# Kernel tuning notes

Measured on AMD Instinct MI355X. Metric: run time of the kernel, lower is better.

The kernel has to match this reference:

```python
import jax, jax.numpy as jnp
import numpy as np

B_SZ, D, HW, STRIDE, HEADS, DK, DV = 32, 64, 64, 4, 2, 32, 32
N = HW * HW                      # 4096 query tokens
M = (HW // STRIDE) ** 2          # 256 key/value tokens
EPS = 1e-5


def setup_inputs() -> dict:
    key = jax.random.key(0)
    ks = jax.random.split(key, 8)
    w = lambda k, s: jax.random.normal(k, s, dtype=jnp.float32) * 0.02
    return {
        "x": jax.random.normal(ks[0], (B_SZ, D, HW, HW), dtype=jnp.float32),
        "W_dw": jax.random.normal(ks[1], (D, 1, STRIDE, STRIDE), dtype=jnp.float32) * 0.1,
        "b_dw": jnp.zeros((D,), jnp.float32),
        "Wq": w(ks[2], (HEADS * DK, D)), "bq": jnp.zeros((HEADS * DK,), jnp.float32),
        "Wk": w(ks[3], (HEADS * DK, D)), "bk": jnp.zeros((HEADS * DK,), jnp.float32),
        "Wv": w(ks[4], (HEADS * DV, D)), "bv": jnp.zeros((HEADS * DV,), jnp.float32),
        "Wo": w(ks[5], (D, HEADS * DV)), "bo": jnp.zeros((D,), jnp.float32),
        "B": jax.random.normal(ks[6], (1, HEADS, N, M), dtype=jnp.float32),
    }


def reference(x, W_dw, b_dw, Wq, bq, Wk, bk, Wv, bv, Wo, bo, B):
    b, c, h, w = x.shape
    heads = B.shape[1]
    dk = Wq.shape[0] // heads
    dv = Wv.shape[0] // heads
    s = W_dw.shape[-1]

    # LayerNorm over (C, H, W), no affine params
    mu = jnp.mean(x, axis=(1, 2, 3), keepdims=True)
    var = jnp.mean((x - mu) ** 2, axis=(1, 2, 3), keepdims=True)
    xn = (x - mu) * jax.lax.rsqrt(var + EPS)

    # Q from normalized input: (b, N, c)
    xr = jnp.transpose(xn.reshape(b, c, h * w), (0, 2, 1))
    q = (xr @ Wq.T + bq).reshape(b, h * w, heads, dk).transpose(0, 2, 1, 3)

    # K/V from depthwise-conv downsample of the *unnormalized* x (as in source)
    kc = jax.lax.conv_general_dilated(
        x, W_dw, window_strides=(s, s), padding="VALID",
        feature_group_count=c,
        dimension_numbers=("NCHW", "OIHW", "NCHW"),
    ) + b_dw[None, :, None, None]
    kh, kw = kc.shape[2], kc.shape[3]
    kv_in = jnp.transpose(kc.reshape(b, c, kh * kw), (0, 2, 1))  # (b, M, c)
    k = (kv_in @ Wk.T + bk).reshape(b, kh * kw, heads, dk).transpose(0, 2, 1, 3)
    v = (kv_in @ Wv.T + bv).reshape(b, kh * kw, heads, dv).transpose(0, 2, 1, 3)

    # Attention with additive relative bias
    attn = jnp.einsum("bhid,bhjd->bhij", q, k) * (dk ** -0.5) + B
    attn = jax.nn.softmax(attn, axis=-1)
    tmp = jnp.einsum("bhij,bhjd->bhid", attn, v)           # (b, heads, N, dv)
    tmp = tmp.transpose(0, 2, 1, 3).reshape(b, h * w, heads * dv)

    # Output proj; NOTE: source does a raw .view(b, d, h, w) (reshape, not permute)
    out = (tmp @ Wo.T + bo).reshape(b, c, h, w)
    return out + x
```

## Files before the change

kernel.cpp:

```cpp
#include <hip/hip_runtime.h>

typedef float f32x4 __attribute__((ext_vector_type(4)));

#define MFMA8(a, b, c) __builtin_amdgcn_mfma_f32_16x16x32_fp8_fp8((long)(a), (long)(b), (c), 0, 0, 0)

__device__ __forceinline__ unsigned char f2fp8(float v) {
    int pk = __builtin_amdgcn_cvt_pk_fp8_f32(v, v, 0, false);
    return (unsigned char)(pk & 0xff);
}
__device__ __forceinline__ long packrow8(const float* p) {
    f32x4 a = *(const f32x4*)(p);
    f32x4 b = *(const f32x4*)(p + 4);
    int lo = __builtin_amdgcn_cvt_pk_fp8_f32(a.x, a.y, 0, false);
    lo = __builtin_amdgcn_cvt_pk_fp8_f32(a.z, a.w, lo, true);
    int hi = __builtin_amdgcn_cvt_pk_fp8_f32(b.x, b.y, 0, false);
    hi = __builtin_amdgcn_cvt_pk_fp8_f32(b.z, b.w, hi, true);
    return (long)(((unsigned long)(unsigned int)hi << 32) | (unsigned int)lo);
}

__global__ __launch_bounds__(256) void k_ln_part(const float* __restrict__ x,
                                                 float* __restrict__ part) {
    const int chunk = blockIdx.x, b = blockIdx.y, t = threadIdx.x;
    const float4* p = (const float4*)(x + b * 262144 + chunk * 16384);
    float s = 0.f, ss = 0.f;
    #pragma unroll
    for (int r = 0; r < 16; ++r) {
        float4 v = p[r * 256 + t];
        s  += v.x + v.y + v.z + v.w;
        ss += v.x * v.x + v.y * v.y + v.z * v.z + v.w * v.w;
    }
    #pragma unroll
    for (int off = 32; off > 0; off >>= 1) {
        s  += __shfl_down(s, off);
        ss += __shfl_down(ss, off);
    }
    __shared__ float sm[8];
    int wv = t >> 6;
    if ((t & 63) == 0) { sm[wv * 2] = s; sm[wv * 2 + 1] = ss; }
    __syncthreads();
    if (t == 0) {
        float S  = sm[0] + sm[2] + sm[4] + sm[6];
        float SS = sm[1] + sm[3] + sm[5] + sm[7];
        part[(b * 16 + chunk) * 2]     = S;
        part[(b * 16 + chunk) * 2 + 1] = SS;
    }
}

__global__ void k_ln_fin(const float* __restrict__ part, float* __restrict__ stats) {
    int t = threadIdx.x;
    if (t < 32) {
        float S = 0.f, SS = 0.f;
        for (int k = 0; k < 16; ++k) {
            S  += part[(t * 16 + k) * 2];
            SS += part[(t * 16 + k) * 2 + 1];
        }
        const float inv = 1.0f / 262144.0f;
        float mu  = S * inv;
        float var = SS * inv - mu * mu;
        stats[t * 2]     = mu;
        stats[t * 2 + 1] = rsqrtf(var + 1e-5f);
    }
}

__global__ __launch_bounds__(512) void k_kvb(
    const float* __restrict__ x, const float* __restrict__ Wdw, const float* __restrict__ bdw,
    const float* __restrict__ Wk, const float* __restrict__ bk,
    const float* __restrict__ Wv, const float* __restrict__ bv,
    unsigned char* __restrict__ Kg, unsigned char* __restrict__ Vg)
{
    __shared__ __align__(16) unsigned char Y[16 * 72];
    const int mi = blockIdx.x, b = blockIdx.y;
    const int t = threadIdx.x, w = t >> 6, lane = t & 63;
    const int quad = lane >> 4, l = lane & 15;
    const float* xb = x + b * 262144;

    const int s2l = lane & 3, mjl = lane >> 2;
    #pragma unroll
    for (int ci = 0; ci < 8; ++ci) {
        int c = w * 8 + ci;
        float wd0 = Wdw[c * 16 + 0 + s2l];
        float wd1 = Wdw[c * 16 + 4 + s2l];
        float wd2 = Wdw[c * 16 + 8 + s2l];
        float wd3 = Wdw[c * 16 + 12 + s2l];
        const float* xr = xb + c * 4096 + mi * 256;
        float acc = xr[lane] * wd0;
        acc = fmaf(xr[64 + lane],  wd1, acc);
        acc = fmaf(xr[128 + lane], wd2, acc);
        acc = fmaf(xr[192 + lane], wd3, acc);
        acc += __shfl_xor(acc, 1);
        acc += __shfl_xor(acc, 2);
        if (s2l == 0) Y[mjl * 72 + c] = f2fp8(acc + bdw[c]);
    }
    __syncthreads();

    long ya0 = *(const long*)(Y + l * 72 + quad * 8);
    long ya1 = *(const long*)(Y + l * 72 + 32 + quad * 8);
    if (w < 4) {
        int e4 = w;
        long f0 = packrow8(Wk + (e4 * 16 + l) * 64 + quad * 8);
        long f1 = packrow8(Wk + (e4 * 16 + l) * 64 + 32 + quad * 8);
        float bb = bk[e4 * 16 + l];
        f32x4 c = { bb, bb, bb, bb };
        c = MFMA8(ya0, f0, c);
        c = MFMA8(ya1, f1, c);
        unsigned char* kd = Kg + b * 16384 + (mi * 16 + quad * 4) * 64 + e4 * 16 + l;
        #pragma unroll
        for (int r = 0; r < 4; ++r) kd[r * 64] = f2fp8(c[r]);
    } else {
        int d4 = w - 4;
        long f0 = packrow8(Wv + (d4 * 16 + l) * 64 + quad * 8);
        long f1 = packrow8(Wv + (d4 * 16 + l) * 64 + 32 + quad * 8);
        f32x4 c = { bv[d4 * 16 + quad * 4 + 0], bv[d4 * 16 + quad * 4 + 1],
                    bv[d4 * 16 + quad * 4 + 2], bv[d4 * 16 + quad * 4 + 3] };
        c = MFMA8(f0, ya0, c);
        c = MFMA8(f1, ya1, c);
        unsigned char* vd = Vg + b * 16384 + (d4 * 16 + quad * 4) * 256 + mi * 16 + l;
        #pragma unroll
        for (int r = 0; r < 4; ++r) vd[r * 256] = f2fp8(c[r]);
    }
}

__global__ __launch_bounds__(512, 4) void k_attn2(
    const float* __restrict__ x, const float* __restrict__ Wq, const float* __restrict__ bq,
    const float* __restrict__ Wo, const float* __restrict__ bo, const float* __restrict__ Bb,
    const float* __restrict__ stats, const unsigned char* __restrict__ Kg,
    const unsigned char* __restrict__ Vg, float* __restrict__ outp)
{
    __shared__ __align__(16) long smem8[7104];
    unsigned char* S = (unsigned char*)smem8;
    unsigned char* Kf = S;
    unsigned char* Vt = S + 20480;
    unsigned char* XS = S + 37888;
    unsigned char* QF = S + 42496;
    unsigned char* TS = S + 52224;
    const int tile = blockIdx.x, b = blockIdx.y;
    const int t = threadIdx.x, w = t >> 6, lane = t & 63;
    const int quad = lane >> 4, l = lane & 15;
    unsigned char* PS = S + 47104 + w * 640;
    const int n0 = tile * 64;
    const float mu = stats[2 * b], rstd = stats[2 * b + 1];
    const float* xb = x + b * 262144;
    const float SCALE = 0.17677669529663687f;

    const unsigned char* Kgb = Kg + b * 16384;
    const unsigned char* Vgb = Vg + b * 16384;
    #pragma unroll
    for (int r = 0; r < 2; ++r) {
        int idx = t + 512 * r;
        int m = idx >> 2, c16 = (idx & 3) * 16;
        *(uint4*)(Kf + m * 80 + c16) = *(const uint4*)(Kgb + m * 64 + c16);
        int d = idx >> 4, e16 = (idx & 15) * 16;
        *(uint4*)(Vt + d * 272 + e16) = *(const uint4*)(Vgb + d * 256 + e16);
    }
    #pragma unroll
    for (int ci = 0; ci < 8; ++ci) {
        int c = w * 8 + ci;
        float v = (xb[c * 4096 + n0 + lane] - mu) * rstd;
        XS[lane * 72 + c] = f2fp8(v);
    }
    const int rtq = w >> 1, ct0 = (w & 1) * 2;
    long wqF[4], woF[4];
    float bqr[2], bor[2];
    #pragma unroll
    for (int i = 0; i < 2; ++i) {
        #pragma unroll
        for (int st = 0; st < 2; ++st) {
            wqF[i * 2 + st] = packrow8(Wq + ((ct0 + i) * 16 + l) * 64 + st * 32 + quad * 8);
            woF[i * 2 + st] = packrow8(Wo + ((ct0 + i) * 16 + l) * 64 + st * 32 + quad * 8);
        }
        bqr[i] = bq[(ct0 + i) * 16 + l];
        bor[i] = bo[(ct0 + i) * 16 + l];
    }
    __syncthreads();

    {
        long xa0 = *(const long*)(XS + (rtq * 16 + l) * 72 + quad * 8);
        long xa1 = *(const long*)(XS + (rtq * 16 + l) * 72 + 32 + quad * 8);
        #pragma unroll
        for (int i = 0; i < 2; ++i) {
            f32x4 c = { bqr[i], bqr[i], bqr[i], bqr[i] };
            c = MFMA8(xa0, wqF[i * 2 + 0], c);
            c = MFMA8(xa1, wqF[i * 2 + 1], c);
            unsigned char* qd = QF + (rtq * 16 + quad * 4) * 72 + (ct0 + i) * 16 + l;
            #pragma unroll
            for (int r = 0; r < 4; ++r) qd[r * 72] = f2fp8(c[r]);
        }
    }
    __syncthreads();

    const int h = w & 1, nq = w >> 1;
    long qa = *(const long*)(QF + (nq * 16 + l) * 72 + h * 32 + quad * 8);
    f32x4 O0 = { 0, 0, 0, 0 }, O1 = { 0, 0, 0, 0 };
    float Lp[4] = { 0, 0, 0, 0 };
    const float* Bbase = Bb + h * 1048576 + (n0 + nq * 16 + quad * 4) * 256;

    #pragma unroll 2
    for (int mc = 0; mc < 8; ++mc) {
        float Bv[2][4];
        #pragma unroll
        for (int sub = 0; sub < 2; ++sub)
            #pragma unroll
            for (int r = 0; r < 4; ++r)
                Bv[sub][r] = Bbase[r * 256 + (mc * 2 + sub) * 16 + l];
        long kb0 = *(const long*)(Kf + ((mc * 2 + 0) * 16 + l) * 80 + h * 32 + quad * 8);
        long kb1 = *(const long*)(Kf + ((mc * 2 + 1) * 16 + l) * 80 + h * 32 + quad * 8);
        #pragma unroll
        for (int sub = 0; sub < 2; ++sub) {
            f32x4 sc = { 0, 0, 0, 0 };
            sc = MFMA8(qa, sub ? kb1 : kb0, sc);
            unsigned char* pw = PS + (quad * 4) * 40 + sub * 16 + l;
            #pragma unroll
            for (int r = 0; r < 4; ++r) {
                float p = __expf(fmaf(sc[r], SCALE, Bv[sub][r]));
                Lp[r] += p;
                pw[r * 40] = f2fp8(p);
            }
        }
        long pa  = *(const long*)(PS + l * 40 + quad * 8);
        long vb0 = *(const long*)(Vt + (h * 32 + l) * 272 + mc * 32 + quad * 8);
        long vb1 = *(const long*)(Vt + (h * 32 + 16 + l) * 272 + mc * 32 + quad * 8);
        O0 = MFMA8(pa, vb0, O0);
        O1 = MFMA8(pa, vb1, O1);
    }
    #pragma unroll
    for (int r = 0; r < 4; ++r) {
        #pragma unroll
        for (int d = 1; d < 16; d <<= 1) Lp[r] += __shfl_xor(Lp[r], d);
    }
    {
        unsigned char* td = TS + (nq * 16 + quad * 4) * 72 + h * 32 + l;
        #pragma unroll
        for (int r = 0; r < 4; ++r) {
            float inv = 1.0f / Lp[r];
            td[r * 72]      = f2fp8(O0[r] * inv);
            td[r * 72 + 16] = f2fp8(O1[r] * inv);
        }
    }
    __syncthreads();

    {
        long ta0 = *(const long*)(TS + (rtq * 16 + l) * 72 + quad * 8);
        long ta1 = *(const long*)(TS + (rtq * 16 + l) * 72 + 32 + quad * 8);
        float* ob = outp + b * 262144 + tile * 4096;
        const float* xr2 = xb + tile * 4096;
        #pragma unroll
        for (int i = 0; i < 2; ++i) {
            f32x4 c = { bor[i], bor[i], bor[i], bor[i] };
            c = MFMA8(ta0, woF[i * 2 + 0], c);
            c = MFMA8(ta1, woF[i * 2 + 1], c);
            #pragma unroll
            for (int r = 0; r < 4; ++r) {
                int off = (rtq * 16 + quad * 4 + r) * 64 + (ct0 + i) * 16 + l;
                ob[off] = c[r] + xr2[off];
            }
        }
    }
}

__global__ __launch_bounds__(512) void k_fused(
    const float* __restrict__ x, const float* __restrict__ Wdw, const float* __restrict__ bdw,
    const float* __restrict__ Wq, const float* __restrict__ bq,
    const float* __restrict__ Wk, const float* __restrict__ bk,
    const float* __restrict__ Wv, const float* __restrict__ bv,
    const float* __restrict__ Wo, const float* __restrict__ bo,
    const float* __restrict__ Bb, const float* __restrict__ stats,
    float* __restrict__ outp)
{
    __shared__ long smem8[6784];
    unsigned char* S = (unsigned char*)smem8;
    unsigned char* Kf = S;
    unsigned char* Vt = S + 18432;
    unsigned char* Y  = S + 35328;
    unsigned char* XS = S + 35328;
    unsigned char* QF = S + 35328 + 4608;
    unsigned char* TS = S + 35328 + 14336;

    const int tg = blockIdx.x, b = blockIdx.y;
    const int t = threadIdx.x, w = t >> 6, lane = t & 63;
    const int quad = lane >> 4, l = lane & 15;
    unsigned char* PS = S + 35328 + 9216 + w * 640;

    const float mu = stats[2 * b], rstd = stats[2 * b + 1];
    const float* xb = x + b * 262144;
    const float SCALE = 0.17677669529663687f;

    long wkF[8], wvF[8];
    #pragma unroll
    for (int e4 = 0; e4 < 4; ++e4)
        #pragma unroll
        for (int st = 0; st < 2; ++st) {
            wkF[e4 * 2 + st] = packrow8(Wk + (e4 * 16 + l) * 64 + st * 32 + quad * 8);
            wvF[e4 * 2 + st] = packrow8(Wv + (e4 * 16 + l) * 64 + st * 32 + quad * 8);
        }
    const int rtq = w >> 1, ct0 = (w & 1) * 2;
    long wqF[4], woF[4];
    #pragma unroll
    for (int i = 0; i < 2; ++i)
        #pragma unroll
        for (int st = 0; st < 2; ++st) {
            wqF[i * 2 + st] = packrow8(Wq + ((ct0 + i) * 16 + l) * 64 + st * 32 + quad * 8);
            woF[i * 2 + st] = packrow8(Wo + ((ct0 + i) * 16 + l) * 64 + st * 32 + quad * 8);
        }
    float bkr[4], bvr[4][4], bqr[2], bor[2];
    #pragma unroll
    for (int e4 = 0; e4 < 4; ++e4) bkr[e4] = bk[e4 * 16 + l];
    #pragma unroll
    for (int d4 = 0; d4 < 4; ++d4)
        #pragma unroll
        for (int r = 0; r < 4; ++r) bvr[d4][r] = bv[d4 * 16 + quad * 4 + r];
    #pragma unroll
    for (int i = 0; i < 2; ++i) { bqr[i] = bq[(ct0 + i) * 16 + l]; bor[i] = bo[(ct0 + i) * 16 + l]; }

    {
        const int s2l = lane & 3, mjl = lane >> 2;
        for (int ci = 0; ci < 8; ++ci) {
            int c = w * 8 + ci;
            float wd0 = Wdw[c * 16 + 0 + s2l];
            float wd1 = Wdw[c * 16 + 4 + s2l];
            float wd2 = Wdw[c * 16 + 8 + s2l];
            float wd3 = Wdw[c * 16 + 12 + s2l];
            float bdc = bdw[c];
            #pragma unroll 4
            for (int mi = 0; mi < 16; ++mi) {
                const float* xr = xb + c * 4096 + mi * 256;
                float acc = xr[lane] * wd0;
                acc = fmaf(xr[64 + lane],  wd1, acc);
                acc = fmaf(xr[128 + lane], wd2, acc);
                acc = fmaf(xr[192 + lane], wd3, acc);
                acc += __shfl_xor(acc, 1);
                acc += __shfl_xor(acc, 2);
                if (s2l == 0) Y[(mi * 16 + mjl) * 72 + c] = f2fp8(acc + bdc);
            }
        }
    }
    __syncthreads();

    #pragma unroll
    for (int i = 0; i < 2; ++i) {
        int rt = w * 2 + i;
        long ya0 = *(const long*)(Y + (rt * 16 + l) * 72 + quad * 8);
        long ya1 = *(const long*)(Y + (rt * 16 + l) * 72 + 32 + quad * 8);
        #pragma unroll
        for (int e4 = 0; e4 < 4; ++e4) {
            f32x4 c = { bkr[e4], bkr[e4], bkr[e4], bkr[e4] };
            c = MFMA8(ya0, wkF[e4 * 2 + 0], c);
            c = MFMA8(ya1, wkF[e4 * 2 + 1], c);
            unsigned char* kd = Kf + (rt * 16 + quad * 4) * 72 + e4 * 16 + l;
            #pragma unroll
            for (int r = 0; r < 4; ++r) kd[r * 72] = f2fp8(c[r]);
        }
        #pragma unroll
        for (int d4 = 0; d4 < 4; ++d4) {
            f32x4 c = { bvr[d4][0], bvr[d4][1], bvr[d4][2], bvr[d4][3] };
            c = MFMA8(wvF[d4 * 2 + 0], ya0, c);
            c = MFMA8(wvF[d4 * 2 + 1], ya1, c);
            unsigned char* vd = Vt + (d4 * 16 + quad * 4) * 264 + rt * 16 + l;
            #pragma unroll
            for (int r = 0; r < 4; ++r) vd[r * 264] = f2fp8(c[r]);
        }
    }
    __syncthreads();

    const int h = w & 1, nq = w >> 1;

    for (int tile = 0; tile < 8; ++tile) {
        const int tidx = tg * 8 + tile, n0 = tidx * 64;

        for (int ci = 0; ci < 8; ++ci) {
            int c = w * 8 + ci;
            float v = (xb[c * 4096 + n0 + lane] - mu) * rstd;
            XS[lane * 72 + c] = f2fp8(v);
        }
        __syncthreads();

        {
            long xa0 = *(const long*)(XS + (rtq * 16 + l) * 72 + quad * 8);
            long xa1 = *(const long*)(XS + (rtq * 16 + l) * 72 + 32 + quad * 8);
            #pragma unroll
            for (int i = 0; i < 2; ++i) {
                f32x4 c = { bqr[i], bqr[i], bqr[i], bqr[i] };
                c = MFMA8(xa0, wqF[i * 2 + 0], c);
                c = MFMA8(xa1, wqF[i * 2 + 1], c);
                unsigned char* qd = QF + (rtq * 16 + quad * 4) * 72 + (ct0 + i) * 16 + l;
                #pragma unroll
                for (int r = 0; r < 4; ++r) qd[r * 72] = f2fp8(c[r]);
            }
        }
        __syncthreads();

        long qa = *(const long*)(QF + (nq * 16 + l) * 72 + h * 32 + quad * 8);
        f32x4 O0 = { 0, 0, 0, 0 }, O1 = { 0, 0, 0, 0 };
        float Lp[4] = { 0, 0, 0, 0 };
        const float* Bbase = Bb + h * 1048576 + (n0 + nq * 16 + quad * 4) * 256;

        #pragma unroll 2
        for (int mc = 0; mc < 8; ++mc) {
            #pragma unroll
            for (int sub = 0; sub < 2; ++sub) {
                int mt = mc * 2 + sub;
                long kb = *(const long*)(Kf + (mt * 16 + l) * 72 + h * 32 + quad * 8);
                f32x4 sc = { 0, 0, 0, 0 };
                sc = MFMA8(qa, kb, sc);
                unsigned char* pw = PS + (quad * 4) * 40 + sub * 16 + l;
                #pragma unroll
                for (int r = 0; r < 4; ++r) {
                    float p = __expf(fmaf(sc[r], SCALE, Bbase[r * 256 + mt * 16 + l]));
                    Lp[r] += p;
                    pw[r * 40] = f2fp8(p);
                }
            }
            long pa  = *(const long*)(PS + l * 40 + quad * 8);
            long vb0 = *(const long*)(Vt + (h * 32 + l) * 264 + mc * 32 + quad * 8);
            long vb1 = *(const long*)(Vt + (h * 32 + 16 + l) * 264 + mc * 32 + quad * 8);
            O0 = MFMA8(pa, vb0, O0);
            O1 = MFMA8(pa, vb1, O1);
        }
        #pragma unroll
        for (int r = 0; r < 4; ++r) {
            #pragma unroll
            for (int d = 1; d < 16; d <<= 1) Lp[r] += __shfl_xor(Lp[r], d);
        }
        {
            unsigned char* td = TS + (nq * 16 + quad * 4) * 72 + h * 32 + l;
            #pragma unroll
            for (int r = 0; r < 4; ++r) {
                float inv = 1.0f / Lp[r];
                td[r * 72]      = f2fp8(O0[r] * inv);
                td[r * 72 + 16] = f2fp8(O1[r] * inv);
            }
        }
        __syncthreads();

        {
            long ta0 = *(const long*)(TS + (rtq * 16 + l) * 72 + quad * 8);
            long ta1 = *(const long*)(TS + (rtq * 16 + l) * 72 + 32 + quad * 8);
            float* ob = outp + b * 262144 + tidx * 4096;
            const float* xr2 = xb + tidx * 4096;
            #pragma unroll
            for (int i = 0; i < 2; ++i) {
                f32x4 c = { bor[i], bor[i], bor[i], bor[i] };
                c = MFMA8(ta0, woF[i * 2 + 0], c);
                c = MFMA8(ta1, woF[i * 2 + 1], c);
                #pragma unroll
                for (int r = 0; r < 4; ++r) {
                    int off = (rtq * 16 + quad * 4 + r) * 64 + (ct0 + i) * 16 + l;
                    ob[off] = c[r] + xr2[off];
                }
            }
        }
        __syncthreads();
    }
}

extern "C" void kernel_launch(void* const* d_in, const int* in_sizes, int n_in,
                              void* d_out, int out_size, void* d_ws, size_t ws_size,
                              hipStream_t stream) {
    (void)in_sizes; (void)n_in; (void)out_size;
    const float* x   = (const float*)d_in[0];
    const float* Wdw = (const float*)d_in[1];
    const float* bdw = (const float*)d_in[2];
    const float* Wq  = (const float*)d_in[3];
    const float* bq  = (const float*)d_in[4];
    const float* Wk  = (const float*)d_in[5];
    const float* bk  = (const float*)d_in[6];
    const float* Wv  = (const float*)d_in[7];
    const float* bv  = (const float*)d_in[8];
    const float* Wo  = (const float*)d_in[9];
    const float* bo  = (const float*)d_in[10];
    const float* Bb  = (const float*)d_in[11];
    float* outp = (float*)d_out;

    float* ws    = (float*)d_ws;
    float* part  = ws;
    float* stats = ws + 1024;
    unsigned char* Kg = (unsigned char*)d_ws + 8192;
    unsigned char* Vg = (unsigned char*)d_ws + 8192 + 524288;

    k_ln_part<<<dim3(16, 32), 256, 0, stream>>>(x, part);
    k_ln_fin<<<1, 64, 0, stream>>>(part, stats);
    if (ws_size >= (size_t)(8192 + 2 * 524288)) {
        k_kvb<<<dim3(16, 32), 512, 0, stream>>>(x, Wdw, bdw, Wk, bk, Wv, bv, Kg, Vg);
        k_attn2<<<dim3(64, 32), 512, 0, stream>>>(x, Wq, bq, Wo, bo, Bb, stats, Kg, Vg, outp);
    } else {
        k_fused<<<dim3(8, 32), 512, 0, stream>>>(x, Wdw, bdw, Wq, bq, Wk, bk, Wv, bv,
                                                 Wo, bo, Bb, stats, outp);
    }
}
```

Measured before the change: 166.7 us.

## Fuse LayerNorm partial sums into KV kernel, pre-quantize weights, prefetch bias

Computes the LayerNorm partial sums inside the depthwise-conv/KV projection kernel, which already reads every element of x, so the separate statistics pass over x is removed. A single-block prep kernel finalizes the statistics and converts Wq/Wo to fp8 once, so attention blocks load packed bytes instead of converting fp32 rows. The attention kernel reuses the XS region for TS to shrink shared memory, raises the occupancy hint, and software-prefetches the next relative-bias chunk. The prefetch adds register pressure, which could cause spills at the higher occupancy target.

```diff
diff --git a/kernel.cpp b/kernel.cpp
--- a/kernel.cpp
+++ b/kernel.cpp
@@ -17,6 +17,10 @@
     hi = __builtin_amdgcn_cvt_pk_fp8_f32(b.z, b.w, hi, true);
     return (long)(((unsigned long)(unsigned int)hi << 32) | (unsigned int)lo);
 }
+__device__ __forceinline__ int pack4(const float* p) {
+    int v = __builtin_amdgcn_cvt_pk_fp8_f32(p[0], p[1], 0, false);
+    return __builtin_amdgcn_cvt_pk_fp8_f32(p[2], p[3], v, true);
+}
 
 __global__ __launch_bounds__(256) void k_ln_part(const float* __restrict__ x,
                                                  float* __restrict__ part) {
@@ -62,19 +66,22 @@
     }
 }
 
-__global__ __launch_bounds__(512) void k_kvb(
+__global__ __launch_bounds__(512) void k_kvb2(
     const float* __restrict__ x, const float* __restrict__ Wdw, const float* __restrict__ bdw,
     const float* __restrict__ Wk, const float* __restrict__ bk,
     const float* __restrict__ Wv, const float* __restrict__ bv,
-    unsigned char* __restrict__ Kg, unsigned char* __restrict__ Vg)
+    unsigned char* __restrict__ Kg, unsigned char* __restrict__ Vg,
+    float* __restrict__ part)
 {
     __shared__ __align__(16) unsigned char Y[16 * 72];
+    __shared__ float sm[16];
     const int mi = blockIdx.x, b = blockIdx.y;
     const int t = threadIdx.x, w = t >> 6, lane = t & 63;
     const int quad = lane >> 4, l = lane & 15;
     const float* xb = x + b * 262144;
 
     const int s2l = lane & 3, mjl = lane >> 2;
+    float s = 0.f, ss = 0.f;
     #pragma unroll
     for (int ci = 0; ci < 8; ++ci) {
         int c = w * 8 + ci;
@@ -83,15 +90,31 @@
         float wd2 = Wdw[c * 16 + 8 + s2l];
         float wd3 = Wdw[c * 16 + 12 + s2l];
         const float* xr = xb + c * 4096 + mi * 256;
-        float acc = xr[lane] * wd0;
-        acc = fmaf(xr[64 + lane],  wd1, acc);
-        acc = fmaf(xr[128 + lane], wd2, acc);
-        acc = fmaf(xr[192 + lane], wd3, acc);
+        float v0 = xr[lane], v1 = xr[64 + lane], v2 = xr[128 + lane], v3 = xr[192 + lane];
+        s  += v0 + v1 + v2 + v3;
+        ss += v0 * v0 + v1 * v1 + v2 * v2 + v3 * v3;
+        float acc = v0 * wd0;
+        acc = fmaf(v1, wd1, acc);
+        acc = fmaf(v2, wd2, acc);
+        acc = fmaf(v3, wd3, acc);
         acc += __shfl_xor(acc, 1);
         acc += __shfl_xor(acc, 2);
         if (s2l == 0) Y[mjl * 72 + c] = f2fp8(acc + bdw[c]);
     }
-    __syncthreads();
+    #pragma unroll
+    for (int off = 32; off > 0; off >>= 1) {
+        s  += __shfl_down(s, off);
+        ss += __shfl_down(ss, off);
+    }
+    if (lane == 0) { sm[w * 2] = s; sm[w * 2 + 1] = ss; }
+    __syncthreads();
+    if (t == 0) {
+        float S = 0.f, SS = 0.f;
+        #pragma unroll
+        for (int i = 0; i < 8; ++i) { S += sm[i * 2]; SS += sm[i * 2 + 1]; }
+        part[(b * 16 + mi) * 2]     = S;
+        part[(b * 16 + mi) * 2 + 1] = SS;
+    }
 
     long ya0 = *(const long*)(Y + l * 72 + quad * 8);
     long ya1 = *(const long*)(Y + l * 72 + 32 + quad * 8);
@@ -120,19 +143,55 @@
     }
 }
 
-__global__ __launch_bounds__(512, 4) void k_attn2(
-    const float* __restrict__ x, const float* __restrict__ Wq, const float* __restrict__ bq,
-    const float* __restrict__ Wo, const float* __restrict__ bo, const float* __restrict__ Bb,
+__global__ void k_prep(const float* __restrict__ part, const float* __restrict__ Wq,
+                       const float* __restrict__ Wo, float* __restrict__ stats,
+                       unsigned char* __restrict__ Wq8, unsigned char* __restrict__ Wo8)
+{
+    int t = threadIdx.x;
+    if (t < 32) {
+        float S = 0.f, SS = 0.f;
+        for (int k = 0; k < 16; ++k) {
+            S  += part[(t * 16 + k) * 2];
+            SS += part[(t * 16 + k) * 2 + 1];
+        }
+        const float inv = 1.0f / 262144.0f;
+        float mu  = S * inv;
+        float var = SS * inv - mu * mu;
+        stats[t * 2]     = mu;
+        stats[t * 2 + 1] = rsqrtf(var + 1e-5f);
+    }
+    {
+        float f[16];
+        #pragma unroll
+        for (int g = 0; g < 4; ++g) *(f32x4*)&f[g * 4] = *(const f32x4*)(Wq + t * 16 + g * 4);
+        uint4 o;
+        o.x = pack4(&f[0]); o.y = pack4(&f[4]); o.z = pack4(&f[8]); o.w = pack4(&f[12]);
+        *(uint4*)(Wq8 + t * 16) = o;
+    }
+    {
+        float f[16];
+        #pragma unroll
+        for (int g = 0; g < 4; ++g) *(f32x4*)&f[g * 4] = *(const f32x4*)(Wo + t * 16 + g * 4);
+        uint4 o;
+        o.x = pack4(&f[0]); o.y = pack4(&f[4]); o.z = pack4(&f[8]); o.w = pack4(&f[12]);
+        *(uint4*)(Wo8 + t * 16) = o;
+    }
+}
+
+__global__ __launch_bounds__(512, 6) void k_attn3(
+    const float* __restrict__ x, const unsigned char* __restrict__ Wq8,
+    const float* __restrict__ bq, const unsigned char* __restrict__ Wo8,
+    const float* __restrict__ bo, const float* __restrict__ Bb,
     const float* __restrict__ stats, const unsigned char* __restrict__ Kg,
     const unsigned char* __restrict__ Vg, float* __restrict__ outp)
 {
-    __shared__ __align__(16) long smem8[7104];
+    __shared__ __align__(16) long smem8[6528];
     unsigned char* S = (unsigned char*)smem8;
     unsigned char* Kf = S;
     unsigned char* Vt = S + 20480;
     unsigned char* XS = S + 37888;
     unsigned char* QF = S + 42496;
-    unsigned char* TS = S + 52224;
+    unsigned char* TS = S + 37888;
     const int tile = blockIdx.x, b = blockIdx.y;
     const int t = threadIdx.x, w = t >> 6, lane = t & 63;
     const int quad = lane >> 4, l = lane & 15;
@@ -165,8 +224,8 @@
     for (int i = 0; i < 2; ++i) {
         #pragma unroll
         for (int st = 0; st < 2; ++st) {
-            wqF[i * 2 + st] = packrow8(Wq + ((ct0 + i) * 16 + l) * 64 + st * 32 + quad * 8);
-            woF[i * 2 + st] = packrow8(Wo + ((ct0 + i) * 16 + l) * 64 + st * 32 + quad * 8);
+            wqF[i * 2 + st] = *(const long*)(Wq8 + ((ct0 + i) * 16 + l) * 64 + st * 32 + quad * 8);
+            woF[i * 2 + st] = *(const long*)(Wo8 + ((ct0 + i) * 16 + l) * 64 + st * 32 + quad * 8);
         }
         bqr[i] = bq[(ct0 + i) * 16 + l];
         bor[i] = bo[(ct0 + i) * 16 + l];
@@ -194,14 +253,23 @@
     float Lp[4] = { 0, 0, 0, 0 };
     const float* Bbase = Bb + h * 1048576 + (n0 + nq * 16 + quad * 4) * 256;
 
+    float Bv[2][4];
+    #pragma unroll
+    for (int sub = 0; sub < 2; ++sub)
+        #pragma unroll
+        for (int r = 0; r < 4; ++r)
+            Bv[sub][r] = Bbase[r * 256 + sub * 16 + l];
+
     #pragma unroll 2
     for (int mc = 0; mc < 8; ++mc) {
-        float Bv[2][4];
-        #pragma unroll
-        for (int sub = 0; sub < 2; ++sub)
-            #pragma unroll
-            for (int r = 0; r < 4; ++r)
-                Bv[sub][r] = Bbase[r * 256 + (mc * 2 + sub) * 16 + l];
+        float Bn[2][4];
+        if (mc < 7) {
+            #pragma unroll
+            for (int sub = 0; sub < 2; ++sub)
+                #pragma unroll
+                for (int r = 0; r < 4; ++r)
+                    Bn[sub][r] = Bbase[r * 256 + (mc * 2 + 2 + sub) * 16 + l];
+        }
         long kb0 = *(const long*)(Kf + ((mc * 2 + 0) * 16 + l) * 80 + h * 32 + quad * 8);
         long kb1 = *(const long*)(Kf + ((mc * 2 + 1) * 16 + l) * 80 + h * 32 + quad * 8);
         #pragma unroll
@@ -221,6 +289,11 @@
         long vb1 = *(const long*)(Vt + (h * 32 + 16 + l) * 272 + mc * 32 + quad * 8);
         O0 = MFMA8(pa, vb0, O0);
         O1 = MFMA8(pa, vb1, O1);
+        #pragma unroll
+        for (int sub = 0; sub < 2; ++sub)
+            #pragma unroll
+            for (int r = 0; r < 4; ++r)
+                Bv[sub][r] = Bn[sub][r];
     }
     #pragma unroll
     for (int r = 0; r < 4; ++r) {
@@ -473,15 +546,18 @@
     float* ws    = (float*)d_ws;
     float* part  = ws;
     float* stats = ws + 1024;
-    unsigned char* Kg = (unsigned char*)d_ws + 8192;
-    unsigned char* Vg = (unsigned char*)d_ws + 8192 + 524288;
-
-    k_ln_part<<<dim3(16, 32), 256, 0, stream>>>(x, part);
-    k_ln_fin<<<1, 64, 0, stream>>>(part, stats);
-    if (ws_size >= (size_t)(8192 + 2 * 524288)) {
-        k_kvb<<<dim3(16, 32), 512, 0, stream>>>(x, Wdw, bdw, Wk, bk, Wv, bv, Kg, Vg);
-        k_attn2<<<dim3(64, 32), 512, 0, stream>>>(x, Wq, bq, Wo, bo, Bb, stats, Kg, Vg, outp);
+    unsigned char* Wq8 = (unsigned char*)d_ws + 8192;
+    unsigned char* Wo8 = (unsigned char*)d_ws + 12288;
+    unsigned char* Kg  = (unsigned char*)d_ws + 16384;
+    unsigned char* Vg  = Kg + 524288;
+
+    if (ws_size >= (size_t)(16384 + 2 * 524288)) {
+        k_kvb2<<<dim3(16, 32), 512, 0, stream>>>(x, Wdw, bdw, Wk, bk, Wv, bv, Kg, Vg, part);
+        k_prep<<<1, 256, 0, stream>>>(part, Wq, Wo, stats, Wq8, Wo8);
+        k_attn3<<<dim3(64, 32), 512, 0, stream>>>(x, Wq8, bq, Wo8, bo, Bb, stats, Kg, Vg, outp);
     } else {
+        k_ln_part<<<dim3(16, 32), 256, 0, stream>>>(x, part);
+        k_ln_fin<<<1, 64, 0, stream>>>(part, stats);
         k_fused<<<dim3(8, 32), 512, 0, stream>>>(x, Wdw, bdw, Wq, bq, Wk, bk, Wv, bv,
                                                  Wo, bo, Bb, stats, outp);
     }
```

New measurement: 145.1 us. 1.15x faster.
